# Performance work log

Hardware: AMD Instinct MI355X
Metric: run time of the kernel (lower is better)

Reference implementation:

```python
import jax, jax.numpy as jnp
import numpy as np

B = 1024     # number of graphs
NMAX = 128   # max nodes per graph (sizes alternate 128/64 -> total 98304 nodes)
D = 128      # feature dim == UOTPooling.dim
NUM = 4      # Bregman-ADMM iterations
EPS = 1e-8
NEG = -1e9   # masked log-value


def setup_inputs() -> dict:
    key = jax.random.key(0)
    ks = jax.random.split(key, 6)
    sizes = np.where(np.arange(B) % 2 == 0, 128, 64)
    batch = jnp.asarray(np.repeat(np.arange(B), sizes), dtype=jnp.int32)  # (98304,)
    T = int(sizes.sum())
    x = jax.random.normal(ks[0], (T, D), dtype=jnp.float32)
    W1 = jax.random.normal(ks[1], (2 * D, D), dtype=jnp.float32) / np.sqrt(D)
    W2 = jax.random.normal(ks[2], (1, 2 * D), dtype=jnp.float32) / np.sqrt(2 * D)
    a1_raw = 0.1 * jax.random.normal(ks[3], (1, 1), dtype=jnp.float32)
    a2_raw = 0.1 * jax.random.normal(ks[4], (1, 1), dtype=jnp.float32)
    a3_raw = 0.1 * jax.random.normal(ks[5], (1, 1), dtype=jnp.float32)
    return {"x": x, "batch": batch, "W1": W1, "W2": W2,
            "a1_raw": a1_raw, "a2_raw": a2_raw, "a3_raw": a3_raw}


def _segment_softmax(scores, batch):
    # torch_geometric.utils.softmax over ragged segments, numerically stable
    m = jax.ops.segment_max(scores, batch, num_segments=B)
    e = jnp.exp(scores - m[batch])
    s = jax.ops.segment_sum(e, batch, num_segments=B)
    return e / (s[batch] + 1e-16)


def _to_dense_batch(v, batch):
    # scatter flat (T, ...) node values into dense (B, NMAX, ...) + validity mask
    T = v.shape[0]
    counts = jax.ops.segment_sum(jnp.ones((T,), jnp.int32), batch, num_segments=B)
    starts = jnp.cumsum(counts) - counts
    pos = jnp.arange(T, dtype=jnp.int32) - starts[batch]
    dense = jnp.zeros((B, NMAX) + v.shape[1:], v.dtype).at[batch, pos].set(v)
    mask = jnp.zeros((B, NMAX), dtype=bool).at[batch, pos].set(True)
    return dense, mask


def _uot_badmm(xd, p0, q0, a1, a2, a3, mask3):
    # log-domain Bregman-ADMM for entropic unbalanced OT ("badmm-e").
    # T: (B, N, D); row marginal (sum over D) ~ eta (samples), column marginal
    # (sum over N) ~ mu (dims); eta, mu softly tied to priors q0, p0 via KL.
    log_p0 = jnp.log(p0 + EPS)                       # (B, 1, D)
    log_q0 = jnp.log(q0 + EPS)                       # (B, N, 1)
    log_t = jnp.where(mask3, log_q0 + log_p0, NEG)   # (B, N, D)
    log_s = log_t
    log_mu = log_p0                                   # (B, 1, D)
    log_eta = jnp.where(mask3, log_q0, NEG)           # (B, N, 1)
    z = jnp.zeros_like(log_t)
    z1 = jnp.zeros_like(log_mu)
    z2 = jnp.zeros_like(log_eta)
    for _ in range(NUM):
        # T-update: each valid row of T sums to eta (softmax over feature dim)
        y = (xd - z) / a1 + log_s
        log_t = jnp.where(mask3, log_eta + jax.nn.log_softmax(y, axis=2), NEG)
        # S-update: each column of S sums to mu (masked softmax over node dim)
        y = jnp.where(mask3, z / a1 + log_t, NEG)
        log_s = jnp.where(mask3, log_mu + jax.nn.log_softmax(y, axis=1), NEG)
        # closed-form KL-prox updates of the unbalanced marginals
        log_cs = jax.scipy.special.logsumexp(log_s, axis=1, keepdims=True)  # (B,1,D)
        log_mu = (a1 * log_cs + a2 * log_p0 - z1) / (a1 + a2)
        log_rt = jax.scipy.special.logsumexp(log_t, axis=2, keepdims=True)  # (B,N,1)
        log_eta = jnp.where(mask3, (a1 * log_rt + a3 * log_q0 - z2) / (a1 + a3), NEG)
        # dual ascent
        z = z + a1 * (jnp.exp(log_t) - jnp.exp(log_s))
        z1 = z1 + a1 * (jnp.exp(log_mu) - jnp.exp(log_cs))
        z2 = z2 + a1 * (jnp.exp(log_eta) - jnp.exp(log_rt))
    return jnp.exp(log_t)


def reference(x, batch, W1, W2, a1_raw, a2_raw, a3_raw):
    # attention scores -> segment softmax -> sample-marginal prior q0
    scores = jnp.tanh(x @ W1.T) @ W2.T               # (T, 1)
    q0_flat = _segment_softmax(scores, batch)        # (T, 1)
    xd, mask = _to_dense_batch(x, batch)             # (B, NMAX, D), (B, NMAX)
    q0, _ = _to_dense_batch(q0_flat, batch)          # (B, NMAX, 1)
    mask3 = mask[:, :, None]                         # (B, NMAX, 1)
    p0 = jnp.full((B, 1, D), 1.0 / D, dtype=x.dtype)
    a1 = jax.nn.softplus(a1_raw)[0, 0]
    a2 = jax.nn.softplus(a2_raw)[0, 0]
    a3 = jax.nn.softplus(a3_raw)[0, 0]
    trans = _uot_badmm(xd, p0, q0, a1, a2, a3, mask3)  # (B, NMAX, D)
    frot = D * xd * trans * mask3
    return jnp.sum(frot, axis=1)                     # (B, D)
```

## Files before the change

kernel.cpp:

```cpp
#include <hip/hip_runtime.h>
#include <math.h>

#define NEGC -1000000000.0f

using f32x2 = __attribute__((ext_vector_type(2))) float;
using f32x4 = __attribute__((ext_vector_type(4))) float;
using s16x8 = __attribute__((ext_vector_type(8))) short;

__device__ __forceinline__ float softplusf(float v){ return log1pf(expf(v)); }
__device__ __forceinline__ short f2bf(float f){
  unsigned u = __float_as_uint(f);
  unsigned r = (u + 0x7fffu + ((u >> 16) & 1u)) >> 16;
  return (short)r;
}
__device__ __forceinline__ float frcp(float v){ return __builtin_amdgcn_rcpf(v); }

__device__ __forceinline__ float addx32(float v){
#if __has_builtin(__builtin_amdgcn_permlane32_swap)
  auto r = __builtin_amdgcn_permlane32_swap(__float_as_uint(v), __float_as_uint(v), false, false);
  return v + __uint_as_float(r[1]);
#else
  return v + __shfl_xor(v, 32, 64);
#endif
}
__device__ __forceinline__ float addx16(float v){
#if __has_builtin(__builtin_amdgcn_permlane16_swap)
  auto r = __builtin_amdgcn_permlane16_swap(__float_as_uint(v), __float_as_uint(v), false, false);
  return v + __uint_as_float(r[1]);
#else
  return v + __shfl_xor(v, 16, 64);
#endif
}
__device__ __forceinline__ float addx8(float v){
  int s = __builtin_amdgcn_update_dpp(0, __float_as_int(v), 0x128, 0xF, 0xF, true);
  return v + __int_as_float(s);
}
__device__ __forceinline__ float addq1(float v){
  int s = __builtin_amdgcn_update_dpp(0, __float_as_int(v), 0xB1, 0xF, 0xF, true);
  return v + __int_as_float(s);
}
__device__ __forceinline__ float addq2(float v){
  int s = __builtin_amdgcn_update_dpp(0, __float_as_int(v), 0x4E, 0xF, 0xF, true);
  return v + __int_as_float(s);
}

__global__ __launch_bounds__(256) void k_prep(const float* __restrict__ W1,
                                              short* __restrict__ wpack,
                                              const int* __restrict__ batch,
                                              int* __restrict__ starts, int T, int Bn,
                                              int* __restrict__ cnt,
                                              int* __restrict__ bigs,
                                              int* __restrict__ smalls){
  const int bx  = blockIdx.x;
  const int tid = threadIdx.x;
  if (bx < 16){
    int gid  = bx * 256 + tid;
    int lane = gid & 63;
    int ft   = gid >> 6;
    int kt   = ft >> 2;
    int dt   = ft & 3;
    const float* src = W1 + (size_t)(kt * 16 + (lane & 15)) * 128 + dt * 32 + (lane >> 4) * 8;
    short o[8];
#pragma unroll
    for (int e = 0; e < 8; ++e) o[e] = f2bf(src[e]);
    *(s16x8*)(wpack + (size_t)gid * 8) = *(const s16x8*)o;
  } else {
    int t = (bx - 16) * 256 + tid;
    if (t > Bn) return;
    int lo = 0, hi = T;
    while (lo < hi){ int mid = (lo + hi) >> 1; if (batch[mid] < t) lo = mid + 1; else hi = mid; }
    if (t == Bn){ starts[Bn] = T; return; }
    starts[t] = lo;
    int lo2 = lo, hi2 = T;
    while (lo2 < hi2){ int mid = (lo2 + hi2) >> 1; if (batch[mid] <= t) lo2 = mid + 1; else hi2 = mid; }
    int nb = lo2 - lo;
    if (nb > 64) bigs[atomicAdd(&cnt[0], 1)] = t;
    else         smalls[atomicAdd(&cnt[1], 1)] = t;
  }
}

__global__ __launch_bounds__(1024)
void k_uot(const float* __restrict__ x,
           const int*   __restrict__ starts,
           const int*   __restrict__ cnt,
           const int*   __restrict__ bigs,
           const int*   __restrict__ smalls,
           const short* __restrict__ wpack,
           const float* __restrict__ W2,
           const float* __restrict__ a1r,
           const float* __restrict__ a2r,
           const float* __restrict__ a3r,
           float* __restrict__ out, int T){
  __shared__ __align__(16) short xs[2 * 64 * 128];
  __shared__ __align__(16) float pbuf[16][164];
  __shared__ float scpart[2][4][64];
  __shared__ float rcsb[2][128];
  __shared__ float lq0s[2][128];
  __shared__ float sred[2][2];

  const int b   = blockIdx.x;
  const int tid = threadIdx.x;
  const int nbig   = cnt[0];
  const int nsmall = cnt[1];

  bool solo; int seg;
  const int half  = tid >> 9;
  const int tid_l = tid & 511;
  if (b < nbig){
    solo = true; seg = bigs[b];
  } else {
    const int i = (b - nbig) * 2 + half;
    solo = false;
    if ((b - nbig) * 2 >= nsmall) return;
    if (i >= nsmall) return;
    seg = smalls[i];
  }

  const int start = starts[seg];
  const int nb    = starts[seg + 1] - start;
  const int hh    = solo ? 0 : half;
  const int tl    = solo ? tid : tid_l;
  const int PL    = solo ? 8 : 4;

  if (nb <= 0){
    if (tl < 128) out[(size_t)seg * 128 + tl] = 0.f;
    return;
  }

  const int n    = tl >> 3;
  const int j    = tl & 7;
  const int wvi  = tid >> 6;
  const int lane = tid & 63;
  const int part = tl & (PL - 1);
  const int col  = tl / PL;
  const int cidx = (col >> 4) * 20 + (col & 15);
  const int wq0  = solo ? 0 : half * 8;
  const int NWh  = solo ? 16 : 8;

  const int u      = tid >> 9;
  const int utid   = tid & 511;
  const int ustart = solo ? (start + u * 64) : start;
#pragma unroll
  for (int itr = 0; itr < 2; ++itr){
    int L  = (itr * 512 + utid) * 8;
    int rr = L >> 7;
    int dc = L & 127;
    int grow = ustart + rr; grow = (grow < T) ? grow : (T - 1);
    const float4 v0 = *(const float4*)(x + (size_t)grow * 128 + dc);
    const float4 v1 = *(const float4*)(x + (size_t)grow * 128 + dc + 4);
    short o[8] = {f2bf(v0.x), f2bf(v0.y), f2bf(v0.z), f2bf(v0.w),
                  f2bf(v1.x), f2bf(v1.y), f2bf(v1.z), f2bf(v1.w)};
    int byte = u * 16384 + rr * 256 + ((dc * 2) ^ ((rr & 7) << 4));
    *(s16x8*)((char*)xs + byte) = *(const s16x8*)o;
  }
  __syncthreads();

  {
    const int lw = wvi & 7;
    const int wm = lw & 1;
    const int wn = lw >> 1;
    f32x4 acc[2][4];
#pragma unroll
    for (int mt = 0; mt < 2; ++mt)
#pragma unroll
      for (int kt = 0; kt < 4; ++kt) acc[mt][kt] = (f32x4){0.f, 0.f, 0.f, 0.f};

    const s16x8* wp = (const s16x8*)wpack;
#pragma unroll
    for (int dt = 0; dt < 4; ++dt){
      s16x8 av[2];
#pragma unroll
      for (int mt = 0; mt < 2; ++mt){
        int arow = wm * 32 + mt * 16 + (lane & 15);
        int byte = u * 16384 + arow * 256 + ((dt * 64 + (lane >> 4) * 16) ^ ((arow & 7) << 4));
        av[mt] = *(const s16x8*)((const char*)xs + byte);
      }
#pragma unroll
      for (int kt = 0; kt < 4; ++kt){
        s16x8 wv = wp[(size_t)((((wn * 4 + kt) * 4 + dt)) << 6) + lane];
#pragma unroll
        for (int mt = 0; mt < 2; ++mt)
          acc[mt][kt] = __builtin_amdgcn_mfma_f32_16x16x32_bf16(av[mt], wv, acc[mt][kt], 0, 0, 0);
      }
    }

    float psum[2][4] = {{0.f,0.f,0.f,0.f},{0.f,0.f,0.f,0.f}};
#pragma unroll
    for (int kt = 0; kt < 4; ++kt){
      const float w2v = W2[(wn * 4 + kt) * 16 + (lane & 15)];
#pragma unroll
      for (int mt = 0; mt < 2; ++mt)
#pragma unroll
        for (int r = 0; r < 4; ++r){
          float e = __expf(2.f * acc[mt][kt][r]);
          psum[mt][r] = fmaf((e - 1.f) * frcp(e + 1.f), w2v, psum[mt][r]);
        }
    }
#pragma unroll
    for (int mt = 0; mt < 2; ++mt)
#pragma unroll
      for (int r = 0; r < 4; ++r){
        float v = psum[mt][r];
        v = addq1(v); v = addq2(v);
        v += __shfl_xor(v, 4, 64); v += __shfl_xor(v, 8, 64);
        if ((lane & 15) == 0)
          scpart[u][wn][wm * 32 + mt * 16 + (lane >> 4) * 4 + r] = v;
      }
  }
  __syncthreads();

  if (tl < 128){
    float sc = NEGC;
    if (tl < nb){
      const int ru = solo ? (tl >> 6) : hh;
      const int rl = tl & 63;
      sc = scpart[ru][0][rl] + scpart[ru][1][rl] + scpart[ru][2][rl] + scpart[ru][3][rl];
    }
    lq0s[hh][tl] = sc;
  }
  __syncthreads();

  if ((wvi & 7) == 0 && (!solo || wvi == 0)){
    float v0 = lq0s[hh][lane], v1 = lq0s[hh][lane + 64];
    float m = fmaxf(v0, v1);
#pragma unroll
    for (int msk = 32; msk; msk >>= 1) m = fmaxf(m, __shfl_xor(m, msk, 64));
    float s = __expf(v0 - m) + __expf(v1 - m);
#pragma unroll
    for (int msk = 32; msk; msk >>= 1) s += __shfl_xor(s, msk, 64);
    if (lane == 0){ sred[hh][0] = m; sred[hh][1] = s; }
  }
  __syncthreads();
  const float smax = sred[hh][0];
  const float rden = frcp(sred[hh][1] + 1e-16f);
  const bool  valid = (n < nb);
  const float lq0 = valid ? __logf(__expf(lq0s[hh][n] - smax) * rden + 1e-8f) : NEGC;

  const float a1 = softplusf(a1r[0]);
  const float a2 = softplusf(a2r[0]);
  const float a3 = softplusf(a3r[0]);
  const float inv_a1 = 1.f / a1;
  const float log_p0 = logf(1.0f / 128.0f + 1e-8f);

  float emu_use[3];
  {
    float z1 = 0.f, lp = log_p0;
    emu_use[0] = __expf(log_p0);
#pragma unroll
    for (int i = 1; i < 3; ++i){
      float nm = (a1 * lp + a2 * log_p0 - z1) / (a1 + a2);
      z1 += a1 * (__expf(nm) - __expf(lp));
      emu_use[i] = __expf(nm); lp = nm;
    }
  }
  float eeta_use[4];
  {
    float z2 = 0.f, lp = lq0;
    eeta_use[0] = __expf(lq0);
#pragma unroll
    for (int i = 1; i < 4; ++i){
      float nm = (a1 * lp + a3 * lq0 - z2) / (a1 + a3);
      z2 += a1 * (__expf(nm) - __expf(lp));
      eeta_use[i] = __expf(nm); lp = nm;
    }
  }

  const int  nc    = valid ? n : (nb - 1);
  const float* xp  = x + (size_t)(start + nc) * 128 + j * 16;
  f32x2 EX2[8], PZ2[8], S2[8];
  {
    const float s0 = __expf(lq0 + log_p0);
#pragma unroll
    for (int p = 0; p < 8; p += 2){
      float4 v = *(const float4*)(xp + p * 2);
      EX2[p]   = (f32x2){__expf(v.x * inv_a1), __expf(v.y * inv_a1)};
      EX2[p+1] = (f32x2){__expf(v.z * inv_a1), __expf(v.w * inv_a1)};
    }
#pragma unroll
    for (int p = 0; p < 8; ++p){ PZ2[p] = (f32x2){1.f, 1.f}; S2[p] = (f32x2){s0, s0}; }
  }

#pragma unroll
  for (int it = 0; it < 4; ++it){
    f32x2 ES2[8];
    f32x2 rs2 = (f32x2){0.f, 0.f};
#pragma unroll
    for (int p = 0; p < 8; ++p){
      ES2[p] = EX2[p] * S2[p];
      rs2 += ES2[p] * PZ2[p];
    }
    float rsum = rs2[0] + rs2[1];
    rsum = addq1(rsum);
    rsum = addq2(rsum);
    rsum += __shfl_xor(rsum, 4, 64);
    const float Et = valid ? (eeta_use[it] * frcp(rsum)) : 0.f;
    const f32x2 Et2 = (f32x2){Et, Et};

    if (it == 3){
      float c[16];
#pragma unroll
      for (int p = 0; p < 8; p += 2){
        float4 v = *(const float4*)(xp + p * 2);
        f32x2 t0 = ES2[p]   * PZ2[p]   * Et2;
        f32x2 t1 = ES2[p+1] * PZ2[p+1] * Et2;
        c[p*2+0] = v.x * t0[0]; c[p*2+1] = v.y * t0[1];
        c[p*2+2] = v.z * t1[0]; c[p*2+3] = v.w * t1[1];
      }
#pragma unroll
      for (int k = 0; k < 16; ++k)
        c[k] = addx8(addx16(addx32(c[k])));
      if (lane < 8){
        float* p = &pbuf[wvi][lane * 20];
        *(float4*)(p + 0)  = make_float4(c[0],  c[1],  c[2],  c[3]);
        *(float4*)(p + 4)  = make_float4(c[4],  c[5],  c[6],  c[7]);
        *(float4*)(p + 8)  = make_float4(c[8],  c[9],  c[10], c[11]);
        *(float4*)(p + 12) = make_float4(c[12], c[13], c[14], c[15]);
      }
      __syncthreads();
      {
        float s = 0.f;
        for (int wq = wq0 + part; wq < wq0 + NWh; wq += PL) s += pbuf[wq][cidx];
        s = addq2(addq1(s));
        if (PL == 8) s += __shfl_xor(s, 4, 64);
        if (part == 0) out[(size_t)seg * 128 + col] = 128.f * s;
      }
    } else {
      const float emu = emu_use[it];
      float c[16];
#pragma unroll
      for (int p = 0; p < 8; ++p){
        f32x2 e2 = ES2[p] * Et2;
        c[p*2+0] = e2[0]; c[p*2+1] = e2[1];
      }
#pragma unroll
      for (int k = 0; k < 16; ++k)
        c[k] = addx8(addx16(addx32(c[k])));
      if (lane < 8){
        float* p = &pbuf[wvi][lane * 20];
        *(float4*)(p + 0)  = make_float4(c[0],  c[1],  c[2],  c[3]);
        *(float4*)(p + 4)  = make_float4(c[4],  c[5],  c[6],  c[7]);
        *(float4*)(p + 8)  = make_float4(c[8],  c[9],  c[10], c[11]);
        *(float4*)(p + 12) = make_float4(c[12], c[13], c[14], c[15]);
      }
      __syncthreads();
      {
        float s = 0.f;
        for (int wq = wq0 + part; wq < wq0 + NWh; wq += PL) s += pbuf[wq][cidx];
        s = addq2(addq1(s));
        if (PL == 8) s += __shfl_xor(s, 4, 64);
        if (part == 0) rcsb[hh][col] = emu * frcp(fmaxf(s, 1e-30f));
      }
      __syncthreads();
      f32x2 rc2[8];
      {
        const float4 r0 = *(const float4*)&rcsb[hh][j * 16 + 0];
        const float4 r1 = *(const float4*)&rcsb[hh][j * 16 + 4];
        const float4 r2 = *(const float4*)&rcsb[hh][j * 16 + 8];
        const float4 r3 = *(const float4*)&rcsb[hh][j * 16 + 12];
        rc2[0] = (f32x2){r0.x, r0.y}; rc2[1] = (f32x2){r0.z, r0.w};
        rc2[2] = (f32x2){r1.x, r1.y}; rc2[3] = (f32x2){r1.z, r1.w};
        rc2[4] = (f32x2){r2.x, r2.y}; rc2[5] = (f32x2){r2.z, r2.w};
        rc2[6] = (f32x2){r3.x, r3.y}; rc2[7] = (f32x2){r3.z, r3.w};
      }
#pragma unroll
      for (int p = 0; p < 8; ++p){
        f32x2 e2  = ES2[p] * Et2;
        f32x2 sn  = e2 * rc2[p];
        f32x2 arg = e2 * (rc2[p] - PZ2[p]);
        PZ2[p] *= (f32x2){__expf(arg[0]), __expf(arg[1])};
        S2[p] = sn;
      }
    }
  }
}

extern "C" void kernel_launch(void* const* d_in, const int* in_sizes, int n_in,
                              void* d_out, int out_size, void* d_ws, size_t ws_size,
                              hipStream_t stream){
  const float* x    = (const float*)d_in[0];
  const int*   batch= (const int*)  d_in[1];
  const float* W1   = (const float*)d_in[2];
  const float* W2   = (const float*)d_in[3];
  const float* a1r  = (const float*)d_in[4];
  const float* a2r  = (const float*)d_in[5];
  const float* a3r  = (const float*)d_in[6];
  float* out = (float*)d_out;

  const int T  = in_sizes[1];
  const int Bn = out_size / 128;

  short* wpack  = (short*)d_ws;
  int*   starts = (int*)(wpack + 32768);
  int*   cnt    = starts + (Bn + 2);
  int*   bigs   = cnt + 2;
  int*   smalls = bigs + Bn;

  hipMemsetAsync(cnt, 0, 2 * sizeof(int), stream);
  const int segBlocks = (Bn + 256) / 256;
  k_prep<<<16 + segBlocks, 256, 0, stream>>>(W1, wpack, batch, starts, T, Bn,
                                             cnt, bigs, smalls);
  k_uot<<<Bn, 1024, 0, stream>>>(x, starts, cnt, bigs, smalls, wpack, W2,
                                 a1r, a2r, a3r, out, T);
}
```

Before: 81.86 us.

## Convert UOT kernel to grid-stride persistent loop over segment work items

The UOT kernel now launches a fixed grid of 512 blocks that loop over work items (one big segment, or a pair of small segments), replacing one block per graph whose tail blocks exited early. The per-block prologue (softplus parameters, emu schedule) is computed once per block instead of once per graph. The change also replaces the hand-written bf16 conversion with the library intrinsic, folds the softmax max reduction so it reads scpart directly and saves one barrier, unrolls the cross-wave partial sum into two loads, and rewrites tanh as 1 - 2/(e+1). In exchange, segments are processed serially inside each block, and inactive halves must still take part in every barrier.

```diff
diff --git a/kernel.cpp b/kernel.cpp
--- a/kernel.cpp
+++ b/kernel.cpp
@@ -1,4 +1,5 @@
 #include <hip/hip_runtime.h>
+#include <hip/hip_bf16.h>
 #include <math.h>
 
 #define NEGC -1000000000.0f
@@ -8,12 +9,11 @@
 using s16x8 = __attribute__((ext_vector_type(8))) short;
 
 __device__ __forceinline__ float softplusf(float v){ return log1pf(expf(v)); }
-__device__ __forceinline__ short f2bf(float f){
-  unsigned u = __float_as_uint(f);
-  unsigned r = (u + 0x7fffu + ((u >> 16) & 1u)) >> 16;
-  return (short)r;
-}
 __device__ __forceinline__ float frcp(float v){ return __builtin_amdgcn_rcpf(v); }
+__device__ __forceinline__ short bfs(float f){
+  __hip_bfloat16 h = __float2bfloat16(f);
+  short s; __builtin_memcpy(&s, &h, 2); return s;
+}
 
 __device__ __forceinline__ float addx32(float v){
 #if __has_builtin(__builtin_amdgcn_permlane32_swap)
@@ -62,7 +62,7 @@
     const float* src = W1 + (size_t)(kt * 16 + (lane & 15)) * 128 + dt * 32 + (lane >> 4) * 8;
     short o[8];
 #pragma unroll
-    for (int e = 0; e < 8; ++e) o[e] = f2bf(src[e]);
+    for (int e = 0; e < 8; ++e) o[e] = bfs(src[e]);
     *(s16x8*)(wpack + (size_t)gid * 8) = *(const s16x8*)o;
   } else {
     int t = (bx - 16) * 256 + tid;
@@ -98,150 +98,22 @@
   __shared__ float lq0s[2][128];
   __shared__ float sred[2][2];
 
-  const int b   = blockIdx.x;
-  const int tid = threadIdx.x;
+  const int tid   = threadIdx.x;
+  const int half  = tid >> 9;
+  const int tid_l = tid & 511;
+  const int wvi   = tid >> 6;
+  const int lane  = tid & 63;
+  const int u     = half;
+
   const int nbig   = cnt[0];
   const int nsmall = cnt[1];
-
-  bool solo; int seg;
-  const int half  = tid >> 9;
-  const int tid_l = tid & 511;
-  if (b < nbig){
-    solo = true; seg = bigs[b];
-  } else {
-    const int i = (b - nbig) * 2 + half;
-    solo = false;
-    if ((b - nbig) * 2 >= nsmall) return;
-    if (i >= nsmall) return;
-    seg = smalls[i];
-  }
-
-  const int start = starts[seg];
-  const int nb    = starts[seg + 1] - start;
-  const int hh    = solo ? 0 : half;
-  const int tl    = solo ? tid : tid_l;
-  const int PL    = solo ? 8 : 4;
-
-  if (nb <= 0){
-    if (tl < 128) out[(size_t)seg * 128 + tl] = 0.f;
-    return;
-  }
-
-  const int n    = tl >> 3;
-  const int j    = tl & 7;
-  const int wvi  = tid >> 6;
-  const int lane = tid & 63;
-  const int part = tl & (PL - 1);
-  const int col  = tl / PL;
-  const int cidx = (col >> 4) * 20 + (col & 15);
-  const int wq0  = solo ? 0 : half * 8;
-  const int NWh  = solo ? 16 : 8;
-
-  const int u      = tid >> 9;
-  const int utid   = tid & 511;
-  const int ustart = solo ? (start + u * 64) : start;
-#pragma unroll
-  for (int itr = 0; itr < 2; ++itr){
-    int L  = (itr * 512 + utid) * 8;
-    int rr = L >> 7;
-    int dc = L & 127;
-    int grow = ustart + rr; grow = (grow < T) ? grow : (T - 1);
-    const float4 v0 = *(const float4*)(x + (size_t)grow * 128 + dc);
-    const float4 v1 = *(const float4*)(x + (size_t)grow * 128 + dc + 4);
-    short o[8] = {f2bf(v0.x), f2bf(v0.y), f2bf(v0.z), f2bf(v0.w),
-                  f2bf(v1.x), f2bf(v1.y), f2bf(v1.z), f2bf(v1.w)};
-    int byte = u * 16384 + rr * 256 + ((dc * 2) ^ ((rr & 7) << 4));
-    *(s16x8*)((char*)xs + byte) = *(const s16x8*)o;
-  }
-  __syncthreads();
-
-  {
-    const int lw = wvi & 7;
-    const int wm = lw & 1;
-    const int wn = lw >> 1;
-    f32x4 acc[2][4];
-#pragma unroll
-    for (int mt = 0; mt < 2; ++mt)
-#pragma unroll
-      for (int kt = 0; kt < 4; ++kt) acc[mt][kt] = (f32x4){0.f, 0.f, 0.f, 0.f};
-
-    const s16x8* wp = (const s16x8*)wpack;
-#pragma unroll
-    for (int dt = 0; dt < 4; ++dt){
-      s16x8 av[2];
-#pragma unroll
-      for (int mt = 0; mt < 2; ++mt){
-        int arow = wm * 32 + mt * 16 + (lane & 15);
-        int byte = u * 16384 + arow * 256 + ((dt * 64 + (lane >> 4) * 16) ^ ((arow & 7) << 4));
-        av[mt] = *(const s16x8*)((const char*)xs + byte);
-      }
-#pragma unroll
-      for (int kt = 0; kt < 4; ++kt){
-        s16x8 wv = wp[(size_t)((((wn * 4 + kt) * 4 + dt)) << 6) + lane];
-#pragma unroll
-        for (int mt = 0; mt < 2; ++mt)
-          acc[mt][kt] = __builtin_amdgcn_mfma_f32_16x16x32_bf16(av[mt], wv, acc[mt][kt], 0, 0, 0);
-      }
-    }
-
-    float psum[2][4] = {{0.f,0.f,0.f,0.f},{0.f,0.f,0.f,0.f}};
-#pragma unroll
-    for (int kt = 0; kt < 4; ++kt){
-      const float w2v = W2[(wn * 4 + kt) * 16 + (lane & 15)];
-#pragma unroll
-      for (int mt = 0; mt < 2; ++mt)
-#pragma unroll
-        for (int r = 0; r < 4; ++r){
-          float e = __expf(2.f * acc[mt][kt][r]);
-          psum[mt][r] = fmaf((e - 1.f) * frcp(e + 1.f), w2v, psum[mt][r]);
-        }
-    }
-#pragma unroll
-    for (int mt = 0; mt < 2; ++mt)
-#pragma unroll
-      for (int r = 0; r < 4; ++r){
-        float v = psum[mt][r];
-        v = addq1(v); v = addq2(v);
-        v += __shfl_xor(v, 4, 64); v += __shfl_xor(v, 8, 64);
-        if ((lane & 15) == 0)
-          scpart[u][wn][wm * 32 + mt * 16 + (lane >> 4) * 4 + r] = v;
-      }
-  }
-  __syncthreads();
-
-  if (tl < 128){
-    float sc = NEGC;
-    if (tl < nb){
-      const int ru = solo ? (tl >> 6) : hh;
-      const int rl = tl & 63;
-      sc = scpart[ru][0][rl] + scpart[ru][1][rl] + scpart[ru][2][rl] + scpart[ru][3][rl];
-    }
-    lq0s[hh][tl] = sc;
-  }
-  __syncthreads();
-
-  if ((wvi & 7) == 0 && (!solo || wvi == 0)){
-    float v0 = lq0s[hh][lane], v1 = lq0s[hh][lane + 64];
-    float m = fmaxf(v0, v1);
-#pragma unroll
-    for (int msk = 32; msk; msk >>= 1) m = fmaxf(m, __shfl_xor(m, msk, 64));
-    float s = __expf(v0 - m) + __expf(v1 - m);
-#pragma unroll
-    for (int msk = 32; msk; msk >>= 1) s += __shfl_xor(s, msk, 64);
-    if (lane == 0){ sred[hh][0] = m; sred[hh][1] = s; }
-  }
-  __syncthreads();
-  const float smax = sred[hh][0];
-  const float rden = frcp(sred[hh][1] + 1e-16f);
-  const bool  valid = (n < nb);
-  const float lq0 = valid ? __logf(__expf(lq0s[hh][n] - smax) * rden + 1e-8f) : NEGC;
+  const int nitems = nbig + ((nsmall + 1) >> 1);
 
   const float a1 = softplusf(a1r[0]);
   const float a2 = softplusf(a2r[0]);
   const float a3 = softplusf(a3r[0]);
   const float inv_a1 = 1.f / a1;
   const float log_p0 = logf(1.0f / 128.0f + 1e-8f);
-
   float emu_use[3];
   {
     float z1 = 0.f, lp = log_p0;
@@ -253,122 +125,249 @@
       emu_use[i] = __expf(nm); lp = nm;
     }
   }
-  float eeta_use[4];
-  {
-    float z2 = 0.f, lp = lq0;
-    eeta_use[0] = __expf(lq0);
-#pragma unroll
-    for (int i = 1; i < 4; ++i){
-      float nm = (a1 * lp + a3 * lq0 - z2) / (a1 + a3);
-      z2 += a1 * (__expf(nm) - __expf(lp));
-      eeta_use[i] = __expf(nm); lp = nm;
-    }
-  }
-
-  const int  nc    = valid ? n : (nb - 1);
-  const float* xp  = x + (size_t)(start + nc) * 128 + j * 16;
-  f32x2 EX2[8], PZ2[8], S2[8];
-  {
-    const float s0 = __expf(lq0 + log_p0);
-#pragma unroll
-    for (int p = 0; p < 8; p += 2){
-      float4 v = *(const float4*)(xp + p * 2);
-      EX2[p]   = (f32x2){__expf(v.x * inv_a1), __expf(v.y * inv_a1)};
-      EX2[p+1] = (f32x2){__expf(v.z * inv_a1), __expf(v.w * inv_a1)};
-    }
-#pragma unroll
-    for (int p = 0; p < 8; ++p){ PZ2[p] = (f32x2){1.f, 1.f}; S2[p] = (f32x2){s0, s0}; }
-  }
-
-#pragma unroll
-  for (int it = 0; it < 4; ++it){
-    f32x2 ES2[8];
-    f32x2 rs2 = (f32x2){0.f, 0.f};
-#pragma unroll
-    for (int p = 0; p < 8; ++p){
-      ES2[p] = EX2[p] * S2[p];
-      rs2 += ES2[p] * PZ2[p];
-    }
-    float rsum = rs2[0] + rs2[1];
-    rsum = addq1(rsum);
-    rsum = addq2(rsum);
-    rsum += __shfl_xor(rsum, 4, 64);
-    const float Et = valid ? (eeta_use[it] * frcp(rsum)) : 0.f;
-    const f32x2 Et2 = (f32x2){Et, Et};
-
-    if (it == 3){
-      float c[16];
+
+  for (int item = blockIdx.x; item < nitems; item += gridDim.x){
+    bool solo; int seg; bool active = true;
+    if (item < nbig){
+      solo = true; seg = bigs[item];
+    } else {
+      solo = false;
+      int i = (item - nbig) * 2 + half;
+      if (i < nsmall) seg = smalls[i];
+      else { seg = smalls[nsmall - 1]; active = false; }
+    }
+    const int start = starts[seg];
+    const int nbr   = starts[seg + 1] - start;
+    const bool haverows = (nbr > 0);
+    const int hh = solo ? 0 : half;
+    const int tl = solo ? tid : tid_l;
+    const int PL = solo ? 8 : 4;
+    if (active && !haverows && tl < 128) out[(size_t)seg * 128 + tl] = 0.f;
+    const bool store_ok = active && haverows;
+
+    const int n    = tl >> 3;
+    const int j    = tl & 7;
+    const int part = tl & (PL - 1);
+    const int col  = tl / PL;
+    const int cidx = (col >> 4) * 20 + (col & 15);
+    const int wq0  = solo ? 0 : half * 8;
+
+    const int ustart = solo ? (start + u * 64) : start;
+#pragma unroll
+    for (int itr = 0; itr < 2; ++itr){
+      int L  = (itr * 512 + tid_l) * 8;
+      int rr = L >> 7;
+      int dc = L & 127;
+      int grow = ustart + rr; grow = (grow < T) ? grow : (T - 1);
+      const float4 v0 = *(const float4*)(x + (size_t)grow * 128 + dc);
+      const float4 v1 = *(const float4*)(x + (size_t)grow * 128 + dc + 4);
+      short o[8] = {bfs(v0.x), bfs(v0.y), bfs(v0.z), bfs(v0.w),
+                    bfs(v1.x), bfs(v1.y), bfs(v1.z), bfs(v1.w)};
+      int byte = u * 16384 + rr * 256 + ((dc * 2) ^ ((rr & 7) << 4));
+      *(s16x8*)((char*)xs + byte) = *(const s16x8*)o;
+    }
+    __syncthreads();
+
+    {
+      const int lw = wvi & 7;
+      const int wm = lw & 1;
+      const int wn = lw >> 1;
+      f32x4 acc[2][4];
+#pragma unroll
+      for (int mt = 0; mt < 2; ++mt)
+#pragma unroll
+        for (int kt = 0; kt < 4; ++kt) acc[mt][kt] = (f32x4){0.f, 0.f, 0.f, 0.f};
+
+      const s16x8* wp = (const s16x8*)wpack;
+#pragma unroll
+      for (int dt = 0; dt < 4; ++dt){
+        s16x8 av[2];
+#pragma unroll
+        for (int mt = 0; mt < 2; ++mt){
+          int arow = wm * 32 + mt * 16 + (lane & 15);
+          int byte = u * 16384 + arow * 256 + ((dt * 64 + (lane >> 4) * 16) ^ ((arow & 7) << 4));
+          av[mt] = *(const s16x8*)((const char*)xs + byte);
+        }
+#pragma unroll
+        for (int kt = 0; kt < 4; ++kt){
+          s16x8 wv = wp[(size_t)((((wn * 4 + kt) * 4 + dt)) << 6) + lane];
+#pragma unroll
+          for (int mt = 0; mt < 2; ++mt)
+            acc[mt][kt] = __builtin_amdgcn_mfma_f32_16x16x32_bf16(av[mt], wv, acc[mt][kt], 0, 0, 0);
+        }
+      }
+
+      float psum[2][4] = {{0.f,0.f,0.f,0.f},{0.f,0.f,0.f,0.f}};
+#pragma unroll
+      for (int kt = 0; kt < 4; ++kt){
+        const float w2v  = W2[(wn * 4 + kt) * 16 + (lane & 15)];
+        const float w2v2 = w2v + w2v;
+#pragma unroll
+        for (int mt = 0; mt < 2; ++mt)
+#pragma unroll
+          for (int r = 0; r < 4; ++r){
+            float e = __expf(2.f * acc[mt][kt][r]);
+            float rc = frcp(e + 1.f);
+            psum[mt][r] = fmaf(-w2v2, rc, psum[mt][r] + w2v);
+          }
+      }
+#pragma unroll
+      for (int mt = 0; mt < 2; ++mt)
+#pragma unroll
+        for (int r = 0; r < 4; ++r){
+          float v = psum[mt][r];
+          v = addq1(v); v = addq2(v);
+          v += __shfl_xor(v, 4, 64); v += __shfl_xor(v, 8, 64);
+          if ((lane & 15) == 0)
+            scpart[u][wn][wm * 32 + mt * 16 + (lane >> 4) * 4 + r] = v;
+        }
+    }
+    __syncthreads();
+
+    float sc = NEGC;
+    if (tl < 128 && tl < nbr){
+      const int ru = solo ? (tl >> 6) : hh;
+      const int rl = tl & 63;
+      sc = scpart[ru][0][rl] + scpart[ru][1][rl] + scpart[ru][2][rl] + scpart[ru][3][rl];
+    }
+    if (tl < 128) lq0s[hh][tl] = sc;
+    if ((wvi & 7) == 0 && (!solo || wvi == 0)){
+      float v1 = NEGC;
+      const int r2 = lane + 64;
+      if (r2 < nbr){
+        const int rl2 = r2 & 63;
+        v1 = scpart[1][0][rl2] + scpart[1][1][rl2] + scpart[1][2][rl2] + scpart[1][3][rl2];
+      }
+      float m = fmaxf(sc, v1);
+#pragma unroll
+      for (int msk = 32; msk; msk >>= 1) m = fmaxf(m, __shfl_xor(m, msk, 64));
+      float s = __expf(sc - m) + __expf(v1 - m);
+#pragma unroll
+      for (int msk = 32; msk; msk >>= 1) s += __shfl_xor(s, msk, 64);
+      if (lane == 0){ sred[hh][0] = m; sred[hh][1] = s; }
+    }
+    __syncthreads();
+    const float smax  = sred[hh][0];
+    const float rden  = frcp(sred[hh][1] + 1e-16f);
+    const bool  valid = haverows && (n < nbr);
+    const float lq0   = valid ? __logf(__expf(lq0s[hh][n] - smax) * rden + 1e-8f) : NEGC;
+
+    float eeta_use[4];
+    {
+      float z2 = 0.f, lp = lq0;
+      eeta_use[0] = __expf(lq0);
+#pragma unroll
+      for (int i = 1; i < 4; ++i){
+        float nm = (a1 * lp + a3 * lq0 - z2) / (a1 + a3);
+        z2 += a1 * (__expf(nm) - __expf(lp));
+        eeta_use[i] = __expf(nm); lp = nm;
+      }
+    }
+
+    const int nc = valid ? n : ((haverows ? nbr : 1) - 1);
+    int xrow = start + nc; if (xrow >= T) xrow = T - 1;
+    const float* xp = x + (size_t)xrow * 128 + j * 16;
+    f32x2 EX2[8], PZ2[8], S2[8];
+    {
+      const float s0 = __expf(lq0 + log_p0);
 #pragma unroll
       for (int p = 0; p < 8; p += 2){
         float4 v = *(const float4*)(xp + p * 2);
-        f32x2 t0 = ES2[p]   * PZ2[p]   * Et2;
-        f32x2 t1 = ES2[p+1] * PZ2[p+1] * Et2;
-        c[p*2+0] = v.x * t0[0]; c[p*2+1] = v.y * t0[1];
-        c[p*2+2] = v.z * t1[0]; c[p*2+3] = v.w * t1[1];
-      }
-#pragma unroll
-      for (int k = 0; k < 16; ++k)
-        c[k] = addx8(addx16(addx32(c[k])));
-      if (lane < 8){
-        float* p = &pbuf[wvi][lane * 20];
-        *(float4*)(p + 0)  = make_float4(c[0],  c[1],  c[2],  c[3]);
-        *(float4*)(p + 4)  = make_float4(c[4],  c[5],  c[6],  c[7]);
-        *(float4*)(p + 8)  = make_float4(c[8],  c[9],  c[10], c[11]);
-        *(float4*)(p + 12) = make_float4(c[12], c[13], c[14], c[15]);
-      }
-      __syncthreads();
-      {
-        float s = 0.f;
-        for (int wq = wq0 + part; wq < wq0 + NWh; wq += PL) s += pbuf[wq][cidx];
-        s = addq2(addq1(s));
-        if (PL == 8) s += __shfl_xor(s, 4, 64);
-        if (part == 0) out[(size_t)seg * 128 + col] = 128.f * s;
-      }
-    } else {
-      const float emu = emu_use[it];
-      float c[16];
+        EX2[p]   = (f32x2){__expf(v.x * inv_a1), __expf(v.y * inv_a1)};
+        EX2[p+1] = (f32x2){__expf(v.z * inv_a1), __expf(v.w * inv_a1)};
+      }
+#pragma unroll
+      for (int p = 0; p < 8; ++p){ PZ2[p] = (f32x2){1.f, 1.f}; S2[p] = (f32x2){s0, s0}; }
+    }
+
+#pragma unroll
+    for (int it = 0; it < 4; ++it){
+      f32x2 ES2[8];
+      f32x2 rs2 = (f32x2){0.f, 0.f};
 #pragma unroll
       for (int p = 0; p < 8; ++p){
-        f32x2 e2 = ES2[p] * Et2;
-        c[p*2+0] = e2[0]; c[p*2+1] = e2[1];
-      }
-#pragma unroll
-      for (int k = 0; k < 16; ++k)
-        c[k] = addx8(addx16(addx32(c[k])));
-      if (lane < 8){
-        float* p = &pbuf[wvi][lane * 20];
-        *(float4*)(p + 0)  = make_float4(c[0],  c[1],  c[2],  c[3]);
-        *(float4*)(p + 4)  = make_float4(c[4],  c[5],  c[6],  c[7]);
-        *(float4*)(p + 8)  = make_float4(c[8],  c[9],  c[10], c[11]);
-        *(float4*)(p + 12) = make_float4(c[12], c[13], c[14], c[15]);
-      }
-      __syncthreads();
-      {
-        float s = 0.f;
-        for (int wq = wq0 + part; wq < wq0 + NWh; wq += PL) s += pbuf[wq][cidx];
-        s = addq2(addq1(s));
-        if (PL == 8) s += __shfl_xor(s, 4, 64);
-        if (part == 0) rcsb[hh][col] = emu * frcp(fmaxf(s, 1e-30f));
-      }
-      __syncthreads();
-      f32x2 rc2[8];
-      {
-        const float4 r0 = *(const float4*)&rcsb[hh][j * 16 + 0];
-        const float4 r1 = *(const float4*)&rcsb[hh][j * 16 + 4];
-        const float4 r2 = *(const float4*)&rcsb[hh][j * 16 + 8];
-        const float4 r3 = *(const float4*)&rcsb[hh][j * 16 + 12];
-        rc2[0] = (f32x2){r0.x, r0.y}; rc2[1] = (f32x2){r0.z, r0.w};
-        rc2[2] = (f32x2){r1.x, r1.y}; rc2[3] = (f32x2){r1.z, r1.w};
-        rc2[4] = (f32x2){r2.x, r2.y}; rc2[5] = (f32x2){r2.z, r2.w};
-        rc2[6] = (f32x2){r3.x, r3.y}; rc2[7] = (f32x2){r3.z, r3.w};
-      }
-#pragma unroll
-      for (int p = 0; p < 8; ++p){
-        f32x2 e2  = ES2[p] * Et2;
-        f32x2 sn  = e2 * rc2[p];
-        f32x2 arg = e2 * (rc2[p] - PZ2[p]);
-        PZ2[p] *= (f32x2){__expf(arg[0]), __expf(arg[1])};
-        S2[p] = sn;
+        ES2[p] = EX2[p] * S2[p];
+        rs2 += ES2[p] * PZ2[p];
+      }
+      float rsum = rs2[0] + rs2[1];
+      rsum = addq1(rsum);
+      rsum = addq2(rsum);
+      rsum += __shfl_xor(rsum, 4, 64);
+      const float Et = valid ? (eeta_use[it] * frcp(rsum)) : 0.f;
+      const f32x2 Et2 = (f32x2){Et, Et};
+
+      if (it == 3){
+        float c[16];
+#pragma unroll
+        for (int p = 0; p < 8; p += 2){
+          float4 v = *(const float4*)(xp + p * 2);
+          f32x2 t0 = ES2[p]   * PZ2[p]   * Et2;
+          f32x2 t1 = ES2[p+1] * PZ2[p+1] * Et2;
+          c[p*2+0] = v.x * t0[0]; c[p*2+1] = v.y * t0[1];
+          c[p*2+2] = v.z * t1[0]; c[p*2+3] = v.w * t1[1];
+        }
+#pragma unroll
+        for (int k = 0; k < 16; ++k)
+          c[k] = addx8(addx16(addx32(c[k])));
+        if (lane < 8){
+          float* p = &pbuf[wvi][lane * 20];
+          *(float4*)(p + 0)  = make_float4(c[0],  c[1],  c[2],  c[3]);
+          *(float4*)(p + 4)  = make_float4(c[4],  c[5],  c[6],  c[7]);
+          *(float4*)(p + 8)  = make_float4(c[8],  c[9],  c[10], c[11]);
+          *(float4*)(p + 12) = make_float4(c[12], c[13], c[14], c[15]);
+        }
+        __syncthreads();
+        {
+          float s = pbuf[wq0 + part][cidx] + pbuf[wq0 + part + PL][cidx];
+          s = addq2(addq1(s));
+          if (PL == 8) s += __shfl_xor(s, 4, 64);
+          if (part == 0 && store_ok) out[(size_t)seg * 128 + col] = 128.f * s;
+        }
+      } else {
+        const float emu = emu_use[it];
+        float c[16];
+#pragma unroll
+        for (int p = 0; p < 8; ++p){
+          f32x2 e2 = ES2[p] * Et2;
+          c[p*2+0] = e2[0]; c[p*2+1] = e2[1];
+        }
+#pragma unroll
+        for (int k = 0; k < 16; ++k)
+          c[k] = addx8(addx16(addx32(c[k])));
+        if (lane < 8){
+          float* p = &pbuf[wvi][lane * 20];
+          *(float4*)(p + 0)  = make_float4(c[0],  c[1],  c[2],  c[3]);
+          *(float4*)(p + 4)  = make_float4(c[4],  c[5],  c[6],  c[7]);
+          *(float4*)(p + 8)  = make_float4(c[8],  c[9],  c[10], c[11]);
+          *(float4*)(p + 12) = make_float4(c[12], c[13], c[14], c[15]);
+        }
+        __syncthreads();
+        {
+          float s = pbuf[wq0 + part][cidx] + pbuf[wq0 + part + PL][cidx];
+          s = addq2(addq1(s));
+          if (PL == 8) s += __shfl_xor(s, 4, 64);
+          if (part == 0) rcsb[hh][col] = emu * frcp(fmaxf(s, 1e-30f));
+        }
+        __syncthreads();
+        f32x2 rc2[8];
+        {
+          const float4 r0 = *(const float4*)&rcsb[hh][j * 16 + 0];
+          const float4 r1 = *(const float4*)&rcsb[hh][j * 16 + 4];
+          const float4 r2 = *(const float4*)&rcsb[hh][j * 16 + 8];
+          const float4 r3 = *(const float4*)&rcsb[hh][j * 16 + 12];
+          rc2[0] = (f32x2){r0.x, r0.y}; rc2[1] = (f32x2){r0.z, r0.w};
+          rc2[2] = (f32x2){r1.x, r1.y}; rc2[3] = (f32x2){r1.z, r1.w};
+          rc2[4] = (f32x2){r2.x, r2.y}; rc2[5] = (f32x2){r2.z, r2.w};
+          rc2[6] = (f32x2){r3.x, r3.y}; rc2[7] = (f32x2){r3.z, r3.w};
+        }
+#pragma unroll
+        for (int p = 0; p < 8; ++p){
+          f32x2 e2  = ES2[p] * Et2;
+          f32x2 sn  = e2 * rc2[p];
+          f32x2 arg = e2 * (rc2[p] - PZ2[p]);
+          PZ2[p] *= (f32x2){__expf(arg[0]), __expf(arg[1])};
+          S2[p] = sn;
+        }
       }
     }
   }
@@ -399,6 +398,6 @@
   const int segBlocks = (Bn + 256) / 256;
   k_prep<<<16 + segBlocks, 256, 0, stream>>>(W1, wpack, batch, starts, T, Bn,
                                              cnt, bigs, smalls);
-  k_uot<<<Bn, 1024, 0, stream>>>(x, starts, cnt, bigs, smalls, wpack, W2,
-                                 a1r, a2r, a3r, out, T);
-}
+  k_uot<<<512, 1024, 0, stream>>>(x, starts, cnt, bigs, smalls, wpack, W2,
+                                  a1r, a2r, a3r, out, T);
+}
```

After: 126.4 us. +54.4%, slower.
